# Kernel tuning notes

Hardware: AMD Instinct MI355X
Metric: run time of the kernel (lower is better)

## Reference

```python
import jax, jax.numpy as jnp
import numpy as np


def setup_inputs() -> dict:
    key = jax.random.key(0)
    x = jax.random.normal(key, (32, 1, 1024, 1024), dtype=jnp.float32)
    return {"x": x}


def reference(x) -> jnp.ndarray:
    # Original torch loop computes a running max down the height dim (dim=2)
    # for channel 0 (C=1 here), overwriting each element with the prefix max.
    # This is exactly a cumulative-max (prefix-max scan) along axis=2.
    return jax.lax.associative_scan(jnp.maximum, x, axis=2)
```

## Files before the change

### kernel.cpp

```cpp
#include <hip/hip_runtime.h>


constexpr int B = 32;
constexpr int H = 1024;
constexpr int W = 1024;
constexpr int ROW4 = W / 4;
constexpr int SW4 = 8;
constexpr int NSTRIP = ROW4 / SW4;
constexpr int CH = 128;
constexpr int NCHUNK = H / CH;
constexpr int R = 4;

__device__ __forceinline__ float4 max4(float4 a, float4 b) {
    return make_float4(fmaxf(a.x, b.x), fmaxf(a.y, b.y),
                       fmaxf(a.z, b.z), fmaxf(a.w, b.w));
}

__device__ __forceinline__ float4 shflup4(float4 v, int d) {
    float4 r;
    r.x = __shfl_up(v.x, d, 64);
    r.y = __shfl_up(v.y, d, 64);
    r.z = __shfl_up(v.z, d, 64);
    r.w = __shfl_up(v.w, d, 64);
    return r;
}

__global__ __launch_bounds__(256) void cummax_sp(const float* __restrict__ xf,
                                                 float* __restrict__ of) {
    __shared__ float4 wavetot[2][32];

    const int tid = threadIdx.x;
    const int lane = tid & 63;
    const int wid = tid >> 6;
    const int w = tid & 7;
    const int hsegG = tid >> 3;
    const int hseg_l = (tid >> 3) & 7;

    const int b = blockIdx.x >> 5;
    const int strip = blockIdx.x & (NSTRIP - 1);
    const float4* x4 = (const float4*)xf;
    float4* o4 = (float4*)of;
    const size_t tbase = (size_t)b * (H * ROW4) + (size_t)strip * SW4 + w;

    const float ninf = -__builtin_inff();
    const float4 ninf4 = make_float4(ninf, ninf, ninf, ninf);
    float4 carry = ninf4;

    float4 cur[R], nxt[R];

#pragma unroll
    for (int r = 0; r < R; ++r)
        cur[r] = x4[tbase + (size_t)(hsegG * R + r) * ROW4];

#pragma unroll
    for (int c = 0; c < NCHUNK; ++c) {
        if (c + 1 < NCHUNK) {
#pragma unroll
            for (int r = 0; r < R; ++r)
                nxt[r] = x4[tbase + (size_t)((c + 1) * CH + hsegG * R + r) * ROW4];
        }

        float4 m = max4(max4(cur[0], cur[1]), max4(cur[2], cur[3]));

        float4 incl = m;
        { float4 t = shflup4(incl, 8);  if (lane >= 8)  incl = max4(incl, t); }
        { float4 t = shflup4(incl, 16); if (lane >= 16) incl = max4(incl, t); }
        { float4 t = shflup4(incl, 32); if (lane >= 32) incl = max4(incl, t); }
        float4 ew = shflup4(incl, 8);
        float4 excl = (hseg_l == 0) ? ninf4 : ew;

        if (hseg_l == 7) wavetot[c & 1][wid * 8 + w] = incl;
        __syncthreads();

        float4 crosspre = carry;
        float4 tot = carry;
#pragma unroll
        for (int w2 = 0; w2 < 4; ++w2) {
            float4 v = wavetot[c & 1][w2 * 8 + w];
            if (w2 < wid) crosspre = max4(crosspre, v);
            tot = max4(tot, v);
        }
        carry = tot;

        float4 a = max4(crosspre, excl);
#pragma unroll
        for (int r = 0; r < R; ++r) {
            a = max4(a, cur[r]);
            o4[tbase + (size_t)(c * CH + hsegG * R + r) * ROW4] = a;
        }

        if (c + 1 < NCHUNK) {
#pragma unroll
            for (int r = 0; r < R; ++r) cur[r] = nxt[r];
        }
    }
}

extern "C" void kernel_launch(void* const* d_in, const int* in_sizes, int n_in,
                              void* d_out, int out_size, void* d_ws, size_t ws_size,
                              hipStream_t stream) {
    const float* x = (const float*)d_in[0];
    float* out = (float*)d_out;
    cummax_sp<<<B * NSTRIP, 256, 0, stream>>>(x, out);
}
```

Measured before the change: 242.3 us.

## Replace block-parallel scan with per-column serial streaming cummax

Replaces the chunked block-wide parallel scan (wave shuffles plus LDS exchange and a barrier per chunk) with single-wave blocks where each lane owns one column and scans the full height serially. Loads are software-prefetched 32 rows ahead into registers, removing all shuffles and synchronization. The trade-off is far fewer waves (512 single-wave blocks), scalar rather than float4 accesses, and a long serial dependency per lane, which may leave memory latency poorly hidden.

```diff
diff --git a/kernel.cpp b/kernel.cpp
--- a/kernel.cpp
+++ b/kernel.cpp
@@ -4,94 +4,48 @@
 constexpr int B = 32;
 constexpr int H = 1024;
 constexpr int W = 1024;
-constexpr int ROW4 = W / 4;
-constexpr int SW4 = 8;
-constexpr int NSTRIP = ROW4 / SW4;
-constexpr int CH = 128;
-constexpr int NCHUNK = H / CH;
-constexpr int R = 4;
+constexpr int SWF = 64;
+constexpr int NSTRIP = W / SWF;
+constexpr int NBLK = B * NSTRIP;
+constexpr int D = 32;
+static_assert(H % D == 0, "D must divide H");
 
-__device__ __forceinline__ float4 max4(float4 a, float4 b) {
-    return make_float4(fmaxf(a.x, b.x), fmaxf(a.y, b.y),
-                       fmaxf(a.z, b.z), fmaxf(a.w, b.w));
-}
+__global__ __launch_bounds__(64) void cummax_stream(const float* __restrict__ x,
+                                                    float* __restrict__ o) {
+    const int sid = blockIdx.x;
+    const int b = sid >> 4;
+    const int st = sid & (NSTRIP - 1);
+    const int lane = threadIdx.x;
 
-__device__ __forceinline__ float4 shflup4(float4 v, int d) {
-    float4 r;
-    r.x = __shfl_up(v.x, d, 64);
-    r.y = __shfl_up(v.y, d, 64);
-    r.z = __shfl_up(v.z, d, 64);
-    r.w = __shfl_up(v.w, d, 64);
-    return r;
-}
+    const size_t base = (size_t)b * H * W + (size_t)st * SWF + lane;
+    const float* xp = x + base;
+    float* op = o + base;
 
-__global__ __launch_bounds__(256) void cummax_sp(const float* __restrict__ xf,
-                                                 float* __restrict__ of) {
-    __shared__ float4 wavetot[2][32];
-
-    const int tid = threadIdx.x;
-    const int lane = tid & 63;
-    const int wid = tid >> 6;
-    const int w = tid & 7;
-    const int hsegG = tid >> 3;
-    const int hseg_l = (tid >> 3) & 7;
-
-    const int b = blockIdx.x >> 5;
-    const int strip = blockIdx.x & (NSTRIP - 1);
-    const float4* x4 = (const float4*)xf;
-    float4* o4 = (float4*)of;
-    const size_t tbase = (size_t)b * (H * ROW4) + (size_t)strip * SW4 + w;
-
-    const float ninf = -__builtin_inff();
-    const float4 ninf4 = make_float4(ninf, ninf, ninf, ninf);
-    float4 carry = ninf4;
-
-    float4 cur[R], nxt[R];
+    float carry = -__builtin_inff();
+    float buf[D];
 
 #pragma unroll
-    for (int r = 0; r < R; ++r)
-        cur[r] = x4[tbase + (size_t)(hsegG * R + r) * ROW4];
+    for (int r = 0; r < D; ++r) buf[r] = xp[(size_t)r * W];
 
+    int hb = 0;
+    for (; hb < H - D; hb += D) {
+        const float* xn = xp + (size_t)(hb + D) * W;
+        float* on = op + (size_t)hb * W;
 #pragma unroll
-    for (int c = 0; c < NCHUNK; ++c) {
-        if (c + 1 < NCHUNK) {
+        for (int r = 0; r < D; ++r) {
+            float v = buf[r];
+            buf[r] = xn[(size_t)r * W];
+            carry = fmaxf(carry, v);
+            on[(size_t)r * W] = carry;
+        }
+    }
+
+    {
+        float* on = op + (size_t)hb * W;
 #pragma unroll
-            for (int r = 0; r < R; ++r)
-                nxt[r] = x4[tbase + (size_t)((c + 1) * CH + hsegG * R + r) * ROW4];
-        }
-
-        float4 m = max4(max4(cur[0], cur[1]), max4(cur[2], cur[3]));
-
-        float4 incl = m;
-        { float4 t = shflup4(incl, 8);  if (lane >= 8)  incl = max4(incl, t); }
-        { float4 t = shflup4(incl, 16); if (lane >= 16) incl = max4(incl, t); }
-        { float4 t = shflup4(incl, 32); if (lane >= 32) incl = max4(incl, t); }
-        float4 ew = shflup4(incl, 8);
-        float4 excl = (hseg_l == 0) ? ninf4 : ew;
-
-        if (hseg_l == 7) wavetot[c & 1][wid * 8 + w] = incl;
-        __syncthreads();
-
-        float4 crosspre = carry;
-        float4 tot = carry;
-#pragma unroll
-        for (int w2 = 0; w2 < 4; ++w2) {
-            float4 v = wavetot[c & 1][w2 * 8 + w];
-            if (w2 < wid) crosspre = max4(crosspre, v);
-            tot = max4(tot, v);
-        }
-        carry = tot;
-
-        float4 a = max4(crosspre, excl);
-#pragma unroll
-        for (int r = 0; r < R; ++r) {
-            a = max4(a, cur[r]);
-            o4[tbase + (size_t)(c * CH + hsegG * R + r) * ROW4] = a;
-        }
-
-        if (c + 1 < NCHUNK) {
-#pragma unroll
-            for (int r = 0; r < R; ++r) cur[r] = nxt[r];
+        for (int r = 0; r < D; ++r) {
+            carry = fmaxf(carry, buf[r]);
+            on[(size_t)r * W] = carry;
         }
     }
 }
@@ -101,5 +55,5 @@
                               hipStream_t stream) {
     const float* x = (const float*)d_in[0];
     float* out = (float*)d_out;
-    cummax_sp<<<B * NSTRIP, 256, 0, stream>>>(x, out);
+    cummax_stream<<<NBLK, 64, 0, stream>>>(x, out);
 }
```

Measured after the change: 235.1 us (median of 3 runs). 3.0% less time.
